# Kernel optimization log

Measured on AMD Instinct MI355X. Metric: run time of the kernel, lower is better.

The kernel has to match this reference:

```python
import jax, jax.numpy as jnp
import numpy as np

D_MODEL = 1024
D_K = 64
B, S = 4, 2048


def setup_inputs() -> dict:
    key = jax.random.key(0)
    k1, k2, k3, k4, k5, k6, k7 = jax.random.split(key, 7)
    return {
        "query": jax.random.normal(k1, (B, S, D_MODEL), dtype=jnp.float32),
        "key": jax.random.normal(k2, (B, S, D_MODEL), dtype=jnp.float32),
        "value": jax.random.normal(k3, (B, S, D_MODEL), dtype=jnp.float32),
        "mask": jax.random.randint(k4, (B, S, S), 0, 2).astype(jnp.bool_),
        # nn.Linear(d_model, d_k, bias=False) weights, stored as [d_k, d_model] like torch
        "w_q": jax.random.normal(k5, (D_K, D_MODEL), dtype=jnp.float32) * (D_MODEL ** -0.5),
        "w_k": jax.random.normal(k6, (D_K, D_MODEL), dtype=jnp.float32) * (D_MODEL ** -0.5),
        "w_v": jax.random.normal(k7, (D_K, D_MODEL), dtype=jnp.float32) * (D_MODEL ** -0.5),
    }


def reference(query, key, value, mask, w_q, w_k, w_v):
    # Linear projections (torch Linear: x @ W.T)
    q = jnp.einsum("bsm,km->bsk", query, w_q)   # [B,S,d_k]
    k = jnp.einsum("bsm,km->bsk", key, w_k)
    v = jnp.einsum("bsm,km->bsk", value, w_v)
    # NOTE: original scales by d_model**-0.5 (not d_k) — keep faithful.
    scores = jnp.einsum("bqk,bsk->bqs", q, k) * (D_MODEL ** -0.5)  # [B,S,S]
    # NOTE: original fills masked positions with 1e-9 (not -inf) BEFORE softmax.
    scores = jnp.where(mask, jnp.float32(1e-9), scores)
    probs = jax.nn.softmax(scores, axis=-1)
    return jnp.einsum("bqs,bsk->bqk", probs, v)  # [B,S,d_k]
```

## Files before the change

kernel.cpp:

```cpp
#include <hip/hip_runtime.h>

#define B_    4
#define S_    2048
#define DM_   1024
#define DK_   64
#define SCALE_ 0.03125f

typedef float        f32x4  __attribute__((ext_vector_type(4)));
typedef float        float8 __attribute__((ext_vector_type(8)));
typedef short        short8 __attribute__((ext_vector_type(8)));
typedef float        fltx4  __attribute__((ext_vector_type(4)));
typedef unsigned int uint2v __attribute__((ext_vector_type(2)));
typedef unsigned int uint4v __attribute__((ext_vector_type(4)));

#define GLL16(gsrc, ldst)                                                   \
  __builtin_amdgcn_global_load_lds(                                         \
      (const __attribute__((address_space(1))) void*)(gsrc),                \
      (__attribute__((address_space(3))) void*)(ldst), 16, 0, 0)

static __device__ __forceinline__ unsigned short f2bf(float f) {
  unsigned u = __float_as_uint(f);
  u += 0x7fffu + ((u >> 16) & 1u);
  return (unsigned short)(u >> 16);
}
static __device__ __forceinline__ uint2v pack4(float a, float b, float c, float d) {
  uint2v r;
  r.x = (unsigned)f2bf(a) | ((unsigned)f2bf(b) << 16);
  r.y = (unsigned)f2bf(c) | ((unsigned)f2bf(d) << 16);
  return r;
}

__global__ void detect_kernel(const unsigned int* __restrict__ m, unsigned int* __restrict__ flag) {
  unsigned v = m[threadIdx.x];
  unsigned long long bad = __ballot(v > 1u);
  if (threadIdx.x == 0) flag[0] = (bad != 0ull) ? 1u : 0u;
}

__global__ __launch_bounds__(256) void wconv_kernel(
    const float* __restrict__ wq, const float* __restrict__ wk, const float* __restrict__ wv,
    unsigned short* __restrict__ Wb)
{
  const int idx   = blockIdx.x * 256 + threadIdx.x;
  const int which = idx >> 13;
  const int e     = idx & 8191;
  const float* __restrict__ w = (which == 0) ? wq : (which == 1) ? wk : wv;
  fltx4 v0 = *reinterpret_cast<const fltx4*>(w + (size_t)e * 8);
  fltx4 v1 = *reinterpret_cast<const fltx4*>(w + (size_t)e * 8 + 4);
  uint4v o;
  o.x = (unsigned)f2bf(v0.x) | ((unsigned)f2bf(v0.y) << 16);
  o.y = (unsigned)f2bf(v0.z) | ((unsigned)f2bf(v0.w) << 16);
  o.z = (unsigned)f2bf(v1.x) | ((unsigned)f2bf(v1.y) << 16);
  o.w = (unsigned)f2bf(v1.z) | ((unsigned)f2bf(v1.w) << 16);
  *reinterpret_cast<uint4v*>(Wb + (size_t)which * 65536 + (size_t)e * 8) = o;
}

__global__ __launch_bounds__(256) void maskpack_kernel(const unsigned char* __restrict__ mb,
                                                       const unsigned int* __restrict__ mi,
                                                       const unsigned int* __restrict__ flag,
                                                       unsigned int* __restrict__ mp) {
  const int w = blockIdx.x * 256 + threadIdx.x;
  unsigned out = 0;
  if (flag[0]) {
    const uint4v* p = reinterpret_cast<const uint4v*>(mb + (size_t)w * 32);
    uint4v a = p[0], b = p[1];
    unsigned ws0[8];
    ws0[0]=a.x; ws0[1]=a.y; ws0[2]=a.z; ws0[3]=a.w; ws0[4]=b.x; ws0[5]=b.y; ws0[6]=b.z; ws0[7]=b.w;
#pragma unroll
    for (int i = 0; i < 8; ++i) {
      unsigned v = ws0[i];
      out |= ((v & 0x000000ffu) ? 1u : 0u) << (i * 4 + 0);
      out |= ((v & 0x0000ff00u) ? 1u : 0u) << (i * 4 + 1);
      out |= ((v & 0x00ff0000u) ? 1u : 0u) << (i * 4 + 2);
      out |= ((v & 0xff000000u) ? 1u : 0u) << (i * 4 + 3);
    }
  } else {
    const uint4v* p = reinterpret_cast<const uint4v*>(mi + (size_t)w * 32);
#pragma unroll
    for (int i = 0; i < 8; ++i) {
      uint4v a = p[i];
      out |= (a.x ? 1u : 0u) << (i * 4 + 0);
      out |= (a.y ? 1u : 0u) << (i * 4 + 1);
      out |= (a.z ? 1u : 0u) << (i * 4 + 2);
      out |= (a.w ? 1u : 0u) << (i * 4 + 3);
    }
  }
  mp[w] = out;
}

__global__ __launch_bounds__(128) void proj6_kernel(
    const float* __restrict__ xq, const float* __restrict__ xk, const float* __restrict__ xv,
    const unsigned short* __restrict__ Wb,
    unsigned short* __restrict__ Qp, unsigned short* __restrict__ Kp, unsigned short* __restrict__ Vt)
{
  const int which = blockIdx.y;
  const float* __restrict__ x = (which == 0) ? xq : (which == 1) ? xk : xv;
  const unsigned short* __restrict__ wsrc = Wb + (size_t)which * 65536;
  const int row0 = blockIdx.x * 32;
  const int tid = threadIdx.x, wid = tid >> 6;
  const int lane = tid & 63, g = lane >> 4, r16 = lane & 15;

  __shared__ __align__(16) float          XsF[4096];
  __shared__ __align__(16) unsigned short WsH[8192];

  f32x4 acc[4];
#pragma unroll
  for (int i = 0; i < 4; ++i) { acc[i].x = 0.f; acc[i].y = 0.f; acc[i].z = 0.f; acc[i].w = 0.f; }

  int xrow[8], xcol[8], wrow[8], wcol[8];
#pragma unroll
  for (int i = 0; i < 8; ++i) {
    int L  = i * 2048 + tid * 16;
    int Ux = L ^ (((L >> 9) & 15) << 4);
    xrow[i] = Ux >> 9;  xcol[i] = (Ux & 511) >> 2;
    int Uw = L ^ (((L >> 8) & 15) << 4);
    wrow[i] = Uw >> 8;  wcol[i] = (Uw & 255) >> 1;
  }

  for (int kb = 0; kb < 8; ++kb) {
    const int k0 = kb * 128;
#pragma unroll
    for (int i = 0; i < 8; ++i)
      GLL16(x + (size_t)(row0 + xrow[i]) * DM_ + k0 + xcol[i],
            (char*)XsF + i * 2048 + wid * 1024);
#pragma unroll
    for (int i = 0; i < 8; ++i)
      GLL16(wsrc + (size_t)wrow[i] * DM_ + k0 + wcol[i],
            (char*)WsH + i * 2048 + wid * 1024);
    __syncthreads();

#pragma unroll
    for (int k2 = 0; k2 < 4; ++k2) {
      const int la  = (wid * 16 + r16) * 512 + k2 * 128 + g * 32;
      const int pa0 = la ^ (r16 << 4);
      const int pa1 = (la + 16) ^ (r16 << 4);
      fltx4 a0 = *reinterpret_cast<const fltx4*>((const char*)XsF + pa0);
      fltx4 a1 = *reinterpret_cast<const fltx4*>((const char*)XsF + pa1);
      short8 a;
      a[0] = (short)f2bf(a0.x); a[1] = (short)f2bf(a0.y);
      a[2] = (short)f2bf(a0.z); a[3] = (short)f2bf(a0.w);
      a[4] = (short)f2bf(a1.x); a[5] = (short)f2bf(a1.y);
      a[6] = (short)f2bf(a1.z); a[7] = (short)f2bf(a1.w);
#pragma unroll
      for (int nf = 0; nf < 4; ++nf) {
        const int lb = (nf * 16 + r16) * 256 + k2 * 64 + g * 16;
        const int pb = lb ^ (r16 << 4);
        short8 b = *reinterpret_cast<const short8*>((const char*)WsH + pb);
        acc[nf] = __builtin_amdgcn_mfma_f32_16x16x32_bf16(a, b, acc[nf], 0, 0, 0);
      }
    }
    __syncthreads();
  }

  if (which < 2) {
    unsigned short* __restrict__ dst = (which == 0) ? Qp : Kp;
#pragma unroll
    for (int nf = 0; nf < 4; ++nf)
#pragma unroll
      for (int j = 0; j < 4; ++j)
        dst[(size_t)(row0 + wid * 16 + g * 4 + j) * DK_ + nf * 16 + r16] = f2bf(acc[nf][j]);
  } else {
    const int grow = row0 + wid * 16 + g * 4;
    const int bb = grow >> 11, sin = grow & 2047;
#pragma unroll
    for (int nf = 0; nf < 4; ++nf)
      *reinterpret_cast<uint2v*>(Vt + (size_t)(bb * DK_ + nf * 16 + r16) * S_ + sin) =
          pack4(acc[nf][0], acc[nf][1], acc[nf][2], acc[nf][3]);
  }
}

__global__ __launch_bounds__(64) void attn_part_kernel(
    const unsigned short* __restrict__ Qp, const unsigned short* __restrict__ Kp,
    const unsigned short* __restrict__ Vt, const unsigned int* __restrict__ mp,
    float* __restrict__ pacc, float* __restrict__ pm, float* __restrict__ pl)
{
  const int lane = threadIdx.x;
  const int g = lane >> 4, r16 = lane & 15;
  const int bx = blockIdx.x;
  const int sp = bx >> 9;
  const int qw = bx & 511;
  const int b  = qw >> 7;
  const int q0 = (qw & 127) * 16;

  __shared__ __align__(16) unsigned short Kt[64][72];
  __shared__ __align__(16) unsigned short Vs[64][72];
  __shared__ __align__(16) unsigned short Pq[16][72];

  short8 aq0, aq1;
  {
    const unsigned short* qrow = Qp + (size_t)(b * S_ + q0 + r16) * DK_ + g * 8;
    aq0 = *reinterpret_cast<const short8*>(qrow);
    aq1 = *reinterpret_cast<const short8*>(qrow + 32);
  }

  float mrun[4], lsum[4], corr[4];
  f32x4 acc[4];
#pragma unroll
  for (int j = 0; j < 4; ++j) { mrun[j] = -3.0e38f; lsum[j] = 0.f; }
#pragma unroll
  for (int nf = 0; nf < 4; ++nf) { acc[nf].x = 0.f; acc[nf].y = 0.f; acc[nf].z = 0.f; acc[nf].w = 0.f; }

  const int srow_stage = lane >> 3, sgran = lane & 7;

  for (int st = sp * 8; st < sp * 8 + 8; ++st) {
    const int s0 = st * 64;
#pragma unroll
    for (int i = 0; i < 8; ++i) {
      int r = i * 8 + srow_stage;
      uint4v kv = *reinterpret_cast<const uint4v*>(Kp + (size_t)(b * S_ + s0 + r) * DK_ + sgran * 8);
      *reinterpret_cast<uint4v*>(&Kt[r][sgran * 8]) = kv;
      uint4v vv = *reinterpret_cast<const uint4v*>(Vt + (size_t)(b * DK_ + r) * S_ + s0 + sgran * 8);
      *reinterpret_cast<uint4v*>(&Vs[r][sgran * 8]) = vv;
    }
    unsigned long long mw[4];
#pragma unroll
    for (int j = 0; j < 4; ++j) {
      size_t widx = ((size_t)(b * S_ + q0 + g * 4 + j) * S_ + s0) >> 5;
      mw[j] = *reinterpret_cast<const unsigned long long*>(mp + widx);
    }
    __syncthreads();

    f32x4 sc[4];
#pragma unroll
    for (int nf = 0; nf < 4; ++nf) { sc[nf].x = 0.f; sc[nf].y = 0.f; sc[nf].z = 0.f; sc[nf].w = 0.f; }
#pragma unroll
    for (int nf = 0; nf < 4; ++nf) {
      short8 bk0 = *reinterpret_cast<const short8*>(&Kt[nf * 16 + r16][g * 8]);
      short8 bk1 = *reinterpret_cast<const short8*>(&Kt[nf * 16 + r16][32 + g * 8]);
      sc[nf] = __builtin_amdgcn_mfma_f32_16x16x32_bf16(aq0, bk0, sc[nf], 0, 0, 0);
      sc[nf] = __builtin_amdgcn_mfma_f32_16x16x32_bf16(aq1, bk1, sc[nf], 0, 0, 0);
    }
#pragma unroll
    for (int nf = 0; nf < 4; ++nf)
#pragma unroll
      for (int j = 0; j < 4; ++j) {
        float v = sc[nf][j] * SCALE_;
        sc[nf][j] = ((mw[j] >> (nf * 16 + r16)) & 1ull) ? 1e-9f : v;
      }
#pragma unroll
    for (int j = 0; j < 4; ++j) {
      float tm = fmaxf(fmaxf(sc[0][j], sc[1][j]), fmaxf(sc[2][j], sc[3][j]));
#pragma unroll
      for (int off = 1; off < 16; off <<= 1) tm = fmaxf(tm, __shfl_xor(tm, off));
      float mn = fmaxf(mrun[j], tm);
      corr[j] = __expf(mrun[j] - mn);
      mrun[j] = mn;
    }
#pragma unroll
    for (int nf = 0; nf < 4; ++nf)
#pragma unroll
      for (int j = 0; j < 4; ++j)
        sc[nf][j] = __expf(sc[nf][j] - mrun[j]);
#pragma unroll
    for (int j = 0; j < 4; ++j) {
      float rs = (sc[0][j] + sc[1][j]) + (sc[2][j] + sc[3][j]);
#pragma unroll
      for (int off = 1; off < 16; off <<= 1) rs += __shfl_xor(rs, off);
      lsum[j] = lsum[j] * corr[j] + rs;
    }
#pragma unroll
    for (int nf = 0; nf < 4; ++nf) {
      acc[nf].x *= corr[0]; acc[nf].y *= corr[1]; acc[nf].z *= corr[2]; acc[nf].w *= corr[3];
    }
#pragma unroll
    for (int nf = 0; nf < 4; ++nf)
#pragma unroll
      for (int j = 0; j < 4; ++j)
        Pq[g * 4 + j][nf * 16 + r16] = f2bf(sc[nf][j]);
    asm volatile("s_waitcnt lgkmcnt(0)" ::: "memory");

#pragma unroll
    for (int k2 = 0; k2 < 2; ++k2) {
      short8 pa = *reinterpret_cast<const short8*>(&Pq[r16][k2 * 32 + g * 8]);
#pragma unroll
      for (int nf = 0; nf < 4; ++nf) {
        short8 bv = *reinterpret_cast<const short8*>(&Vs[nf * 16 + r16][k2 * 32 + g * 8]);
        acc[nf] = __builtin_amdgcn_mfma_f32_16x16x32_bf16(pa, bv, acc[nf], 0, 0, 0);
      }
    }
    __syncthreads();
  }

  float* __restrict__ pa = pacc + (size_t)(sp * 512 + qw) * 1024;
#pragma unroll
  for (int nf = 0; nf < 4; ++nf)
#pragma unroll
    for (int j = 0; j < 4; ++j)
      pa[(g * 4 + j) * 64 + nf * 16 + r16] = acc[nf][j];
  if (r16 == 0) {
#pragma unroll
    for (int j = 0; j < 4; ++j) {
      pm[(sp * 512 + qw) * 16 + g * 4 + j] = mrun[j];
      pl[(sp * 512 + qw) * 16 + g * 4 + j] = lsum[j];
    }
  }
}

__global__ __launch_bounds__(64) void attn_merge_kernel(
    const float* __restrict__ pacc, const float* __restrict__ pm, const float* __restrict__ pl,
    float* __restrict__ out)
{
  const int qw = blockIdx.x;
  const int b = qw >> 7, q0 = (qw & 127) * 16;
  const int lane = threadIdx.x;

#pragma unroll 1
  for (int row = 0; row < 16; ++row) {
    float m0 = pm[(0 * 512 + qw) * 16 + row], m1 = pm[(1 * 512 + qw) * 16 + row];
    float m2 = pm[(2 * 512 + qw) * 16 + row], m3 = pm[(3 * 512 + qw) * 16 + row];
    float M = fmaxf(fmaxf(m0, m1), fmaxf(m2, m3));
    float w0 = __expf(m0 - M), w1 = __expf(m1 - M), w2 = __expf(m2 - M), w3 = __expf(m3 - M);
    float L = w0 * pl[(0 * 512 + qw) * 16 + row] + w1 * pl[(1 * 512 + qw) * 16 + row] +
              w2 * pl[(2 * 512 + qw) * 16 + row] + w3 * pl[(3 * 512 + qw) * 16 + row];
    float v = w0 * pacc[((size_t)(0 * 512 + qw) * 16 + row) * 64 + lane] +
              w1 * pacc[((size_t)(1 * 512 + qw) * 16 + row) * 64 + lane] +
              w2 * pacc[((size_t)(2 * 512 + qw) * 16 + row) * 64 + lane] +
              w3 * pacc[((size_t)(3 * 512 + qw) * 16 + row) * 64 + lane];
    out[(size_t)(b * S_ + q0 + row) * DK_ + lane] = v / L;
  }
}

__global__ __launch_bounds__(64) void attn_kernel(
    const unsigned short* __restrict__ Qp, const unsigned short* __restrict__ Kp,
    const unsigned short* __restrict__ Vt, const unsigned int* __restrict__ mp,
    float* __restrict__ out)
{
  const int lane = threadIdx.x;
  const int g = lane >> 4, r16 = lane & 15;
  const int qt = blockIdx.x & 127;
  const int b  = blockIdx.x >> 7;
  const int q0 = qt * 16;

  __shared__ __align__(16) unsigned short Kt[64][72];
  __shared__ __align__(16) unsigned short Vs[64][72];
  __shared__ __align__(16) unsigned short Pq[16][72];

  short8 aq0, aq1;
  {
    const unsigned short* qrow = Qp + (size_t)(b * S_ + q0 + r16) * DK_ + g * 8;
    aq0 = *reinterpret_cast<const short8*>(qrow);
    aq1 = *reinterpret_cast<const short8*>(qrow + 32);
  }

  float mrun[4], lsum[4], corr[4];
  f32x4 acc[4];
#pragma unroll
  for (int j = 0; j < 4; ++j) { mrun[j] = -3.0e38f; lsum[j] = 0.f; }
#pragma unroll
  for (int nf = 0; nf < 4; ++nf) { acc[nf].x = 0.f; acc[nf].y = 0.f; acc[nf].z = 0.f; acc[nf].w = 0.f; }

  const int srow_stage = lane >> 3, sgran = lane & 7;

  for (int st = 0; st < 32; ++st) {
    const int s0 = st * 64;
#pragma unroll
    for (int i = 0; i < 8; ++i) {
      int r = i * 8 + srow_stage;
      uint4v kv = *reinterpret_cast<const uint4v*>(Kp + (size_t)(b * S_ + s0 + r) * DK_ + sgran * 8);
      *reinterpret_cast<uint4v*>(&Kt[r][sgran * 8]) = kv;
      uint4v vv = *reinterpret_cast<const uint4v*>(Vt + (size_t)(b * DK_ + r) * S_ + s0 + sgran * 8);
      *reinterpret_cast<uint4v*>(&Vs[r][sgran * 8]) = vv;
    }
    unsigned long long mw[4];
#pragma unroll
    for (int j = 0; j < 4; ++j) {
      size_t widx = ((size_t)(b * S_ + q0 + g * 4 + j) * S_ + s0) >> 5;
      mw[j] = *reinterpret_cast<const unsigned long long*>(mp + widx);
    }
    __syncthreads();

    f32x4 sc[4];
#pragma unroll
    for (int nf = 0; nf < 4; ++nf) { sc[nf].x = 0.f; sc[nf].y = 0.f; sc[nf].z = 0.f; sc[nf].w = 0.f; }
#pragma unroll
    for (int nf = 0; nf < 4; ++nf) {
      short8 bk0 = *reinterpret_cast<const short8*>(&Kt[nf * 16 + r16][g * 8]);
      short8 bk1 = *reinterpret_cast<const short8*>(&Kt[nf * 16 + r16][32 + g * 8]);
      sc[nf] = __builtin_amdgcn_mfma_f32_16x16x32_bf16(aq0, bk0, sc[nf], 0, 0, 0);
      sc[nf] = __builtin_amdgcn_mfma_f32_16x16x32_bf16(aq1, bk1, sc[nf], 0, 0, 0);
    }
#pragma unroll
    for (int nf = 0; nf < 4; ++nf)
#pragma unroll
      for (int j = 0; j < 4; ++j) {
        float v = sc[nf][j] * SCALE_;
        sc[nf][j] = ((mw[j] >> (nf * 16 + r16)) & 1ull) ? 1e-9f : v;
      }
#pragma unroll
    for (int j = 0; j < 4; ++j) {
      float tm = fmaxf(fmaxf(sc[0][j], sc[1][j]), fmaxf(sc[2][j], sc[3][j]));
#pragma unroll
      for (int off = 1; off < 16; off <<= 1) tm = fmaxf(tm, __shfl_xor(tm, off));
      float mn = fmaxf(mrun[j], tm);
      corr[j] = __expf(mrun[j] - mn);
      mrun[j] = mn;
    }
#pragma unroll
    for (int nf = 0; nf < 4; ++nf)
#pragma unroll
      for (int j = 0; j < 4; ++j)
        sc[nf][j] = __expf(sc[nf][j] - mrun[j]);
#pragma unroll
    for (int j = 0; j < 4; ++j) {
      float rs = (sc[0][j] + sc[1][j]) + (sc[2][j] + sc[3][j]);
#pragma unroll
      for (int off = 1; off < 16; off <<= 1) rs += __shfl_xor(rs, off);
      lsum[j] = lsum[j] * corr[j] + rs;
    }
#pragma unroll
    for (int nf = 0; nf < 4; ++nf) {
      acc[nf].x *= corr[0]; acc[nf].y *= corr[1]; acc[nf].z *= corr[2]; acc[nf].w *= corr[3];
    }
#pragma unroll
    for (int nf = 0; nf < 4; ++nf)
#pragma unroll
      for (int j = 0; j < 4; ++j)
        Pq[g * 4 + j][nf * 16 + r16] = f2bf(sc[nf][j]);
    asm volatile("s_waitcnt lgkmcnt(0)" ::: "memory");

#pragma unroll
    for (int k2 = 0; k2 < 2; ++k2) {
      short8 pa = *reinterpret_cast<const short8*>(&Pq[r16][k2 * 32 + g * 8]);
#pragma unroll
      for (int nf = 0; nf < 4; ++nf) {
        short8 bv = *reinterpret_cast<const short8*>(&Vs[nf * 16 + r16][k2 * 32 + g * 8]);
        acc[nf] = __builtin_amdgcn_mfma_f32_16x16x32_bf16(pa, bv, acc[nf], 0, 0, 0);
      }
    }
    __syncthreads();
  }

#pragma unroll
  for (int nf = 0; nf < 4; ++nf)
#pragma unroll
    for (int j = 0; j < 4; ++j)
      out[(size_t)(b * S_ + q0 + g * 4 + j) * DK_ + nf * 16 + r16] = acc[nf][j] / lsum[j];
}

extern "C" void kernel_launch(void* const* d_in, const int* in_sizes, int n_in,
                              void* d_out, int out_size, void* d_ws, size_t ws_size,
                              hipStream_t stream) {
  const float* q  = (const float*)d_in[0];
  const float* k  = (const float*)d_in[1];
  const float* v  = (const float*)d_in[2];
  const void*  mk = d_in[3];
  const float* wq = (const float*)d_in[4];
  const float* wk = (const float*)d_in[5];
  const float* wv = (const float*)d_in[6];

  char* ws = (char*)d_ws;
  unsigned short* Qp   = (unsigned short*)(ws);
  unsigned short* Kp   = (unsigned short*)(ws + (1u << 20));
  unsigned short* Vt   = (unsigned short*)(ws + (2u << 20));
  unsigned int*   mp   = (unsigned int*)  (ws + (3u << 20));
  unsigned int*   flag = (unsigned int*)  (ws + (5u << 20));
  unsigned short* Wb   = (unsigned short*)(ws + (5u << 20) + 4096);
  float*          pacc = (float*)(ws + (6u << 20));
  float*          pm   = (float*)(ws + (14u << 20));
  float*          pl   = (float*)(ws + (14u << 20) + (1u << 17));

  wconv_kernel<<<96, 256, 0, stream>>>(wq, wk, wv, Wb);
  detect_kernel<<<1, 64, 0, stream>>>((const unsigned int*)mk, flag);
  maskpack_kernel<<<2048, 256, 0, stream>>>((const unsigned char*)mk, (const unsigned int*)mk, flag, mp);
  proj6_kernel<<<dim3(256, 3), 128, 0, stream>>>(q, k, v, Wb, Qp, Kp, Vt);

  if (ws_size >= (15u << 20)) {
    attn_part_kernel<<<2048, 64, 0, stream>>>(Qp, Kp, Vt, mp, pacc, pm, pl);
    attn_merge_kernel<<<512, 64, 0, stream>>>(pacc, pm, pl, (float*)d_out);
  } else {
    attn_kernel<<<512, 64, 0, stream>>>(Qp, Kp, Vt, mp, (float*)d_out);
  }
}
```

Baseline: 86.16 us.

## Halve projection row tile, split output columns across waves, remap attention block order

The projection kernel now handles 16 rows per block instead of 32, so it launches twice as many blocks (512x3). Each of the two waves computes half of the 64 output columns for the same rows rather than separate row groups, which raises parallelism and halves the X tile in LDS. The cost is that each weight tile is reloaded by twice as many blocks. The attention partial kernel also remaps block indices so that neighbouring block IDs go to different split/query groups, which changes how work is spread across CUs and XCDs.

```diff
diff --git a/kernel.cpp b/kernel.cpp
--- a/kernel.cpp
+++ b/kernel.cpp
@@ -87,7 +87,7 @@
   mp[w] = out;
 }
 
-__global__ __launch_bounds__(128) void proj6_kernel(
+__global__ __launch_bounds__(128) void proj7_kernel(
     const float* __restrict__ xq, const float* __restrict__ xk, const float* __restrict__ xv,
     const unsigned short* __restrict__ Wb,
     unsigned short* __restrict__ Qp, unsigned short* __restrict__ Kp, unsigned short* __restrict__ Vt)
@@ -95,23 +95,27 @@
   const int which = blockIdx.y;
   const float* __restrict__ x = (which == 0) ? xq : (which == 1) ? xk : xv;
   const unsigned short* __restrict__ wsrc = Wb + (size_t)which * 65536;
-  const int row0 = blockIdx.x * 32;
+  const int row0 = blockIdx.x * 16;
   const int tid = threadIdx.x, wid = tid >> 6;
   const int lane = tid & 63, g = lane >> 4, r16 = lane & 15;
 
-  __shared__ __align__(16) float          XsF[4096];
+  __shared__ __align__(16) float          XsF[2048];
   __shared__ __align__(16) unsigned short WsH[8192];
 
-  f32x4 acc[4];
-#pragma unroll
-  for (int i = 0; i < 4; ++i) { acc[i].x = 0.f; acc[i].y = 0.f; acc[i].z = 0.f; acc[i].w = 0.f; }
-
-  int xrow[8], xcol[8], wrow[8], wcol[8];
-#pragma unroll
-  for (int i = 0; i < 8; ++i) {
+  f32x4 acc[2];
+#pragma unroll
+  for (int i = 0; i < 2; ++i) { acc[i].x = 0.f; acc[i].y = 0.f; acc[i].z = 0.f; acc[i].w = 0.f; }
+
+  int xrow[4], xcol[4], wrow[8], wcol[8];
+#pragma unroll
+  for (int i = 0; i < 4; ++i) {
     int L  = i * 2048 + tid * 16;
     int Ux = L ^ (((L >> 9) & 15) << 4);
     xrow[i] = Ux >> 9;  xcol[i] = (Ux & 511) >> 2;
+  }
+#pragma unroll
+  for (int i = 0; i < 8; ++i) {
+    int L  = i * 2048 + tid * 16;
     int Uw = L ^ (((L >> 8) & 15) << 4);
     wrow[i] = Uw >> 8;  wcol[i] = (Uw & 255) >> 1;
   }
@@ -119,7 +123,7 @@
   for (int kb = 0; kb < 8; ++kb) {
     const int k0 = kb * 128;
 #pragma unroll
-    for (int i = 0; i < 8; ++i)
+    for (int i = 0; i < 4; ++i)
       GLL16(x + (size_t)(row0 + xrow[i]) * DM_ + k0 + xcol[i],
             (char*)XsF + i * 2048 + wid * 1024);
 #pragma unroll
@@ -130,7 +134,7 @@
 
 #pragma unroll
     for (int k2 = 0; k2 < 4; ++k2) {
-      const int la  = (wid * 16 + r16) * 512 + k2 * 128 + g * 32;
+      const int la  = r16 * 512 + k2 * 128 + g * 32;
       const int pa0 = la ^ (r16 << 4);
       const int pa1 = (la + 16) ^ (r16 << 4);
       fltx4 a0 = *reinterpret_cast<const fltx4*>((const char*)XsF + pa0);
@@ -141,8 +145,9 @@
       a[4] = (short)f2bf(a1.x); a[5] = (short)f2bf(a1.y);
       a[6] = (short)f2bf(a1.z); a[7] = (short)f2bf(a1.w);
 #pragma unroll
-      for (int nf = 0; nf < 4; ++nf) {
-        const int lb = (nf * 16 + r16) * 256 + k2 * 64 + g * 16;
+      for (int nf = 0; nf < 2; ++nf) {
+        const int nfe = wid * 2 + nf;
+        const int lb = (nfe * 16 + r16) * 256 + k2 * 64 + g * 16;
         const int pb = lb ^ (r16 << 4);
         short8 b = *reinterpret_cast<const short8*>((const char*)WsH + pb);
         acc[nf] = __builtin_amdgcn_mfma_f32_16x16x32_bf16(a, b, acc[nf], 0, 0, 0);
@@ -154,17 +159,21 @@
   if (which < 2) {
     unsigned short* __restrict__ dst = (which == 0) ? Qp : Kp;
 #pragma unroll
-    for (int nf = 0; nf < 4; ++nf)
+    for (int nf = 0; nf < 2; ++nf) {
+      const int nfe = wid * 2 + nf;
 #pragma unroll
       for (int j = 0; j < 4; ++j)
-        dst[(size_t)(row0 + wid * 16 + g * 4 + j) * DK_ + nf * 16 + r16] = f2bf(acc[nf][j]);
+        dst[(size_t)(row0 + g * 4 + j) * DK_ + nfe * 16 + r16] = f2bf(acc[nf][j]);
+    }
   } else {
-    const int grow = row0 + wid * 16 + g * 4;
+    const int grow = row0 + g * 4;
     const int bb = grow >> 11, sin = grow & 2047;
 #pragma unroll
-    for (int nf = 0; nf < 4; ++nf)
-      *reinterpret_cast<uint2v*>(Vt + (size_t)(bb * DK_ + nf * 16 + r16) * S_ + sin) =
+    for (int nf = 0; nf < 2; ++nf) {
+      const int nfe = wid * 2 + nf;
+      *reinterpret_cast<uint2v*>(Vt + (size_t)(bb * DK_ + nfe * 16 + r16) * S_ + sin) =
           pack4(acc[nf][0], acc[nf][1], acc[nf][2], acc[nf][3]);
+    }
   }
 }
 
@@ -176,8 +185,9 @@
   const int lane = threadIdx.x;
   const int g = lane >> 4, r16 = lane & 15;
   const int bx = blockIdx.x;
-  const int sp = bx >> 9;
-  const int qw = bx & 511;
+  const int bxl = (bx & 7) * 256 + (bx >> 3);
+  const int sp = bxl >> 9;
+  const int qw = bxl & 511;
   const int b  = qw >> 7;
   const int q0 = (qw & 127) * 16;
 
@@ -461,7 +471,7 @@
   wconv_kernel<<<96, 256, 0, stream>>>(wq, wk, wv, Wb);
   detect_kernel<<<1, 64, 0, stream>>>((const unsigned int*)mk, flag);
   maskpack_kernel<<<2048, 256, 0, stream>>>((const unsigned char*)mk, (const unsigned int*)mk, flag, mp);
-  proj6_kernel<<<dim3(256, 3), 128, 0, stream>>>(q, k, v, Wb, Qp, Kp, Vt);
+  proj7_kernel<<<dim3(512, 3), 128, 0, stream>>>(q, k, v, Wb, Qp, Kp, Vt);
 
   if (ws_size >= (15u << 20)) {
     attn_part_kernel<<<2048, 64, 0, stream>>>(Qp, Kp, Vt, mp, pacc, pm, pl);
```

After: 88.80 us. 1.03x slower.
